# Optimization experiments

Measured on AMD Instinct MI355X. Metric: run time of the kernel, lower is better.

## Reference

```python
import jax, jax.numpy as jnp
import numpy as np

HX_INIT = 1e-6  # matches torch: zeros + 1e-06


def log_g(x):
    # log of continuous activation g: x>=0 -> log(x+0.5), else log(sigmoid(x)) = -softplus(-x)
    return jnp.where(x >= 0, jnp.log(jax.nn.relu(x) + 0.5), -jax.nn.softplus(-x))


def setup_inputs() -> dict:
    key = jax.random.key(0)
    k1, k2, k3 = jax.random.split(key, 3)
    N, L, H_in, H = 8, 4096, 512, 512
    x = jax.random.normal(k1, (N, L, H_in), dtype=jnp.float32)
    W = jax.random.normal(k2, (3 * H, H_in), dtype=jnp.float32) * 0.05
    b = jax.random.normal(k3, (3 * H,), dtype=jnp.float32) * 0.05
    return {"x": x, "W": W, "b": b}


def reference(x, W, b):
    N, L, _ = x.shape
    H = W.shape[0] // 3
    # gate preactivations: (N, L, 3H)
    pre = jnp.einsum('nli,oi->nlo', x, W) + b
    f_pre, i_pre, h_pre = jnp.split(pre, 3, axis=-1)
    # log-space gates
    diff = jax.nn.softplus(-f_pre) - jax.nn.softplus(-i_pre)
    log_f = -jax.nn.softplus(diff)       # log f'_t
    log_i = -jax.nn.softplus(-diff)      # log i'_t
    log_tilde_h = log_g(h_pre)
    # initial hidden state hx = 1e-6 (zeros + eps), shape (N, 1, H)
    log_h0 = jnp.full((N, 1, H), jnp.log(jnp.asarray(HX_INIT, x.dtype)), dtype=x.dtype)
    log_values = jnp.concatenate([log_h0, log_i + log_tilde_h], axis=1)  # (N, L+1, H)
    # Heinsen log-space parallel scan
    a_star = jnp.pad(jnp.cumsum(log_f, axis=1), ((0, 0), (1, 0), (0, 0)))  # (N, L+1, H)
    log_h = a_star + jax.lax.cumlogsumexp(log_values - a_star, axis=1)
    return jnp.exp(log_h)[:, 1:]  # (N, L, H)
```

## Files before the change

### kernel.cpp

```cpp
#include <hip/hip_runtime.h>
#include <hip/hip_bf16.h>


#define H_DIM 512
#define LSEQ 4096
#define NBATCH 8
#define M_TOTAL (NBATCH * LSEQ)

#define BM 128
#define BK 64

#define CS 128
#define NC 32

typedef __attribute__((ext_vector_type(8))) short short8;
typedef __attribute__((ext_vector_type(4))) float floatx4;
typedef __attribute__((ext_vector_type(4))) float float4v;
typedef _Float16 h2 __attribute__((ext_vector_type(2)));
typedef _Float16 h4 __attribute__((ext_vector_type(4)));
typedef __attribute__((ext_vector_type(2))) float float2v;

#define NEG_BIG (-1.0e30f)
#define C_LOG2E 1.4426950408889634f
#define LOG2_HX0 (-19.931568569324174f)

__device__ __forceinline__ float exp2_hw(float x) {
#if __has_builtin(__builtin_amdgcn_exp2f)
    return __builtin_amdgcn_exp2f(x);
#else
    return exp2f(x);
#endif
}

__device__ __forceinline__ float log2_hw(float x) {
#if __has_builtin(__builtin_amdgcn_logf)
    return __builtin_amdgcn_logf(x);
#else
    return log2f(x);
#endif
}

__device__ __forceinline__ float logaddexp2_f(float p, float q) {
    float m = fmaxf(p, q);
    float d = -fabsf(p - q);
    return m + log2_hw(1.0f + exp2_hw(d));
}

__device__ __forceinline__ float bf16u_to_f(unsigned short u) {
    unsigned int w = ((unsigned int)u) << 16;
    float f;
    __builtin_memcpy(&f, &w, 4);
    return f;
}

__device__ __forceinline__ unsigned short f_to_bf16u(float f) {
    __hip_bfloat16 h = __float2bfloat16(f);
    unsigned short u;
    __builtin_memcpy(&u, &h, 2);
    return u;
}

__device__ __forceinline__ void gload_lds16(const void* g, void* l) {
    __builtin_amdgcn_global_load_lds(
        (const __attribute__((address_space(1))) unsigned int*)g,
        (__attribute__((address_space(3))) unsigned int*)l, 16, 0, 0);
}

__global__ void detect_and_bias(const unsigned short* __restrict__ xu,
                                const void* __restrict__ bsrc,
                                int* __restrict__ flag,
                                float* __restrict__ bdst) {
    __shared__ int cnt;
    if (threadIdx.x == 0) cnt = 0;
    __syncthreads();
    int local = 0;
    for (int i = threadIdx.x; i < 16384; i += 256) {
        unsigned short u = xu[i];
        if (((u >> 7) & 0xFF) == 0xFF) local++;
    }
    if (local) atomicAdd(&cnt, local);
    __syncthreads();
    int f = (cnt > 8) ? 1 : 0;
    if (threadIdx.x == 0) flag[0] = f;
    for (int i = threadIdx.x; i < 3 * H_DIM; i += 256)
        bdst[i] = f ? ((const float*)bsrc)[i]
                    : bf16u_to_f(((const unsigned short*)bsrc)[i]);
}

__global__ __launch_bounds__(256)
void convert_inputs(const void* __restrict__ x, const void* __restrict__ W,
                    unsigned short* __restrict__ xc,
                    unsigned short* __restrict__ Wc,
                    const int* __restrict__ flag) {
    const int bx = blockIdx.x;
    const void* src;
    unsigned short* dst;
    int i;
    if (bx < 8192) { src = x; dst = xc; i = (bx * 256 + threadIdx.x) * 8; }
    else           { src = W; dst = Wc; i = ((bx - 8192) * 256 + threadIdx.x) * 8; }
    if (*flag) {
        const float4v* s4 = (const float4v*)((const float*)src + i);
        float4v a = s4[0], b = s4[1];
        short8 v;
        v[0] = (short)f_to_bf16u(a[0]); v[1] = (short)f_to_bf16u(a[1]);
        v[2] = (short)f_to_bf16u(a[2]); v[3] = (short)f_to_bf16u(a[3]);
        v[4] = (short)f_to_bf16u(b[0]); v[5] = (short)f_to_bf16u(b[1]);
        v[6] = (short)f_to_bf16u(b[2]); v[7] = (short)f_to_bf16u(b[3]);
        *(short8*)&dst[i] = v;
    } else {
        *(short8*)&dst[i] = *(const short8*)&((const short*)src)[i];
    }
}

__global__ __launch_bounds__(256, 3)
void gemm_gates(const unsigned short* __restrict__ x,
                const unsigned short* __restrict__ W,
                const float* __restrict__ bias,
                h2* __restrict__ plv,
                float* __restrict__ Asum, float* __restrict__ Bval,
                float* __restrict__ Asub, float* __restrict__ Bsub) {
    __shared__ __align__(16) char ldsbuf[40960];
    short* Alds = (short*)ldsbuf;
    short* Blds = (short*)(ldsbuf + 16384);
    h2* sc = (h2*)ldsbuf;
    float* sa = (float*)(ldsbuf + 32768);
    float* sb = sa + 256;

    const int bx = blockIdx.x;
    const int by = blockIdx.y;
    const int tid = threadIdx.x;
    const int lane = tid & 63;
    const int w = tid >> 6;
    const int wr = (w >> 1) * 64;
    const int wc2 = w & 1;
    const int l8 = lane >> 3, s8 = lane & 7;
    const int sg = s8 ^ l8;
    const int fr = lane & 15;
    const int q = lane >> 4;

    const int R0 = by * BM;

    floatx4 acc[4][6];
    #pragma unroll
    for (int i = 0; i < 4; i++)
        #pragma unroll
        for (int j = 0; j < 6; j++)
            acc[i][j] = (floatx4){0.f, 0.f, 0.f, 0.f};

    const short* xg = (const short*)x;
    const short* wg = (const short*)W;

    for (int k0 = 0; k0 < H_DIM; k0 += BK) {
        __syncthreads();
        #pragma unroll
        for (int i = 0; i < 4; i++) {
            int c = w * 4 + i;
            const short* g = xg + (size_t)(R0 + c * 8 + l8) * H_DIM + k0 + sg * 8;
            gload_lds16(g, &Alds[c * 512]);
        }
        #pragma unroll
        for (int i = 0; i < 6; i++) {
            int c = w * 6 + i;
            int br = c * 8 + l8;
            int wrow = (br >> 6) * H_DIM + bx * 64 + (br & 63);
            const short* g = wg + (size_t)wrow * H_DIM + k0 + sg * 8;
            gload_lds16(g, &Blds[c * 512]);
        }
        __syncthreads();

        #pragma unroll
        for (int ks = 0; ks < 2; ks++) {
            const int s = ks * 4 + q;
            short8 af[4], bf[6];
            #pragma unroll
            for (int mt = 0; mt < 4; mt++) {
                int ar = wr + mt * 16 + fr;
                af[mt] = *(const short8*)&Alds[ar * BK + ((s ^ (ar & 7)) << 3)];
            }
            #pragma unroll
            for (int j = 0; j < 6; j++) {
                int nt = (j >> 1) * 4 + wc2 * 2 + (j & 1);
                int brr = nt * 16 + fr;
                bf[j] = *(const short8*)&Blds[brr * BK + ((s ^ (brr & 7)) << 3)];
            }
            #pragma unroll
            for (int mt = 0; mt < 4; mt++)
                #pragma unroll
                for (int j = 0; j < 6; j++)
                    acc[mt][j] = __builtin_amdgcn_mfma_f32_16x16x32_bf16(
                        af[mt], bf[j], acc[mt][j], 0, 0, 0);
        }
    }

    __syncthreads();

    const int rowb = R0 + wr + q * 4;
    const int tloc0 = wr + q * 4;
    #pragma unroll
    for (int jj = 0; jj < 2; jj++) {
        int hl = wc2 * 32 + jj * 16 + fr;
        int hcol = bx * 64 + hl;
        float bfv = bias[hcol];
        float biv = bias[H_DIM + hcol];
        float bhv = bias[2 * H_DIM + hcol];
        float bf2 = -bfv * C_LOG2E;
        float bi2 = -biv * C_LOG2E;
        #pragma unroll
        for (int mt = 0; mt < 4; mt++) {
            #pragma unroll
            for (int r = 0; r < 4; r++) {
                float ef = exp2_hw(fminf(fmaf(acc[mt][jj][r], -C_LOG2E, bf2), 126.0f));
                float ei = exp2_hw(fminf(fmaf(acc[mt][2 + jj][r], -C_LOG2E, bi2), 126.0f));
                float hp = acc[mt][4 + jj][r] + bhv;
                float eh = exp2_hw(fminf(-hp * C_LOG2E, 126.0f));
                float afv = 1.0f + ef, aiv = 1.0f + ei;
                float sfi = afv + aiv;
                float ls = log2_hw(sfi);
                float lf = log2_hw(aiv) - ls;
                float marg = (hp >= 0.0f) ? (hp + 0.5f) : (1.0f + eh);
                float lm = log2_hw(marg);
                float lg = (hp >= 0.0f) ? lm : -lm;
                float lv = (log2_hw(afv) - ls) + lg;
                int row = rowb + mt * 16 + r;
                h2 pk;
                pk[0] = (_Float16)lf;
                pk[1] = (_Float16)lv;
                plv[(size_t)row * H_DIM + hcol] = pk;
                sc[(tloc0 + mt * 16 + r) * 64 + hl] = pk;
            }
        }
    }

    __syncthreads();

    const int n = by >> 5, c = by & 31;
    {
        float a = 0.f, bacc = NEG_BIG;
        const int t0 = w * 32;
        #pragma unroll 4
        for (int t = t0; t < t0 + 32; t++) {
            h2 p = sc[t * 64 + lane];
            float f = (float)p[0];
            bacc = logaddexp2_f(f + bacc, (float)p[1]);
            a += f;
        }
        sa[w * 64 + lane] = a;
        sb[w * 64 + lane] = bacc;
        size_t o = (((size_t)n * NC + c) * 4 + w) * H_DIM + bx * 64 + lane;
        Asub[o] = a;
        Bsub[o] = bacc;
    }
    __syncthreads();

    if (w == 0) {
        float a = sa[lane], b = sb[lane];
        #pragma unroll
        for (int s = 1; s < 4; s++) {
            float as = sa[s * 64 + lane], bs = sb[s * 64 + lane];
            b = logaddexp2_f(as + b, bs);
            a += as;
        }
        size_t o = ((size_t)n * NC + c) * H_DIM + bx * 64 + lane;
        Asum[o] = a;
        Bval[o] = b;
    }
}

__global__ __launch_bounds__(256)
void scan_apply(const h2* __restrict__ plv,
                const float* __restrict__ Asum, const float* __restrict__ Bval,
                const float* __restrict__ Asub, const float* __restrict__ Bsub,
                void* __restrict__ outv, const int* __restrict__ flag) {
    const int cc = blockIdx.x;
    const int n = blockIdx.y;
    const int c = cc >> 2, s = cc & 3;
    const int h0 = threadIdx.x * 2;
    const int f32out = *flag;

    float r0 = LOG2_HX0;
    float r1 = r0;
    size_t so = (size_t)n * NC * H_DIM + h0;
    int cp = 0;
    for (; cp + 4 <= c; cp += 4) {
        float2v A0 = *(const float2v*)&Asum[so + (size_t)(cp + 0) * H_DIM];
        float2v B0 = *(const float2v*)&Bval[so + (size_t)(cp + 0) * H_DIM];
        float2v A1 = *(const float2v*)&Asum[so + (size_t)(cp + 1) * H_DIM];
        float2v B1 = *(const float2v*)&Bval[so + (size_t)(cp + 1) * H_DIM];
        float2v A2 = *(const float2v*)&Asum[so + (size_t)(cp + 2) * H_DIM];
        float2v B2 = *(const float2v*)&Bval[so + (size_t)(cp + 2) * H_DIM];
        float2v A3 = *(const float2v*)&Asum[so + (size_t)(cp + 3) * H_DIM];
        float2v B3 = *(const float2v*)&Bval[so + (size_t)(cp + 3) * H_DIM];
        r0 = logaddexp2_f(A0[0] + r0, B0[0]); r1 = logaddexp2_f(A0[1] + r1, B0[1]);
        r0 = logaddexp2_f(A1[0] + r0, B1[0]); r1 = logaddexp2_f(A1[1] + r1, B1[1]);
        r0 = logaddexp2_f(A2[0] + r0, B2[0]); r1 = logaddexp2_f(A2[1] + r1, B2[1]);
        r0 = logaddexp2_f(A3[0] + r0, B3[0]); r1 = logaddexp2_f(A3[1] + r1, B3[1]);
    }
    for (; cp < c; cp++) {
        float2v A = *(const float2v*)&Asum[so + (size_t)cp * H_DIM];
        float2v B = *(const float2v*)&Bval[so + (size_t)cp * H_DIM];
        r0 = logaddexp2_f(A[0] + r0, B[0]);
        r1 = logaddexp2_f(A[1] + r1, B[1]);
    }
    size_t sub = (((size_t)n * NC + c) * 4) * H_DIM + h0;
    for (int sp = 0; sp < s; sp++) {
        float2v A = *(const float2v*)&Asub[sub + (size_t)sp * H_DIM];
        float2v B = *(const float2v*)&Bsub[sub + (size_t)sp * H_DIM];
        r0 = logaddexp2_f(A[0] + r0, B[0]);
        r1 = logaddexp2_f(A[1] + r1, B[1]);
    }

    size_t base = ((size_t)n * LSEQ + (size_t)c * CS + s * 32) * H_DIM + h0;
    if (f32out) {
        float* of = (float*)outv;
        #pragma unroll 4
        for (int t = 0; t < 32; t++) {
            size_t idx = base + (size_t)t * H_DIM;
            h4 p = *(const h4*)&plv[idx];
            r0 = logaddexp2_f((float)p[0] + r0, (float)p[1]);
            r1 = logaddexp2_f((float)p[2] + r1, (float)p[3]);
            float2v o2 = {exp2_hw(r0), exp2_hw(r1)};
            *(float2v*)&of[idx] = o2;
        }
    } else {
        unsigned int* ob32 = (unsigned int*)outv;
        #pragma unroll 4
        for (int t = 0; t < 32; t++) {
            size_t idx = base + (size_t)t * H_DIM;
            h4 p = *(const h4*)&plv[idx];
            r0 = logaddexp2_f((float)p[0] + r0, (float)p[1]);
            r1 = logaddexp2_f((float)p[2] + r1, (float)p[3]);
            unsigned int pk = ((unsigned int)f_to_bf16u(exp2_hw(r1)) << 16)
                            | f_to_bf16u(exp2_hw(r0));
            ob32[idx >> 1] = pk;
        }
    }
}

extern "C" void kernel_launch(void* const* d_in, const int* in_sizes, int n_in,
                              void* d_out, int out_size, void* d_ws, size_t ws_size,
                              hipStream_t stream) {
    const void* x = d_in[0];
    const void* W = d_in[1];
    const void* b = d_in[2];

    char* wsb = (char*)d_ws;
    int* flag            = (int*)wsb;
    float* bconv         = (float*)(wsb + 16);
    unsigned short* xc   = (unsigned short*)(wsb + 16384);
    unsigned short* Wc   = (unsigned short*)(wsb + 16384 + 33554432);
    h2* plv              = (h2*)(wsb + 36700160);
    float* Asum          = (float*)(wsb + 103809024);
    float* Bval          = (float*)(wsb + 104333312);
    float* Asub          = (float*)(wsb + 104857600);
    float* Bsub          = (float*)(wsb + 106954752);

    detect_and_bias<<<1, 256, 0, stream>>>((const unsigned short*)x, b, flag, bconv);
    convert_inputs<<<8576, 256, 0, stream>>>(x, W, xc, Wc, flag);

    dim3 g1(H_DIM / 64, M_TOTAL / BM);
    gemm_gates<<<g1, 256, 0, stream>>>(xc, Wc, bconv, plv, Asum, Bval, Asub, Bsub);

    dim3 g2(NC * 4, NBATCH);
    scan_apply<<<g2, 256, 0, stream>>>(plv, Asum, Bval, Asub, Bsub, d_out, flag);
}
```

Baseline: 235.6 us.

## Fuse fp32-to-bf16 conversion of x into GEMM A-tile loads

Drops the separate pass that converted x to bf16. When the input is fp32, the GEMM now reads fp32 x directly, packs it to bf16 with v_cvt_pk_bf16_f32 and stores the result into LDS; only W is still converted ahead of time. This removes a full write and re-read of the converted activation buffer. The grid axes are also swapped so consecutive blocks walk along rows instead of output columns. That changes L2 reuse: x is now fetched as fp32 once per column tile, and the A loads become synchronous register loads instead of direct-to-LDS loads.

Result: no change. 238.4 us (+1.2%).

```diff
diff --git a/kernel.cpp b/kernel.cpp
--- a/kernel.cpp
+++ b/kernel.cpp
@@ -60,6 +60,12 @@
     return u;
 }
 
+__device__ __forceinline__ unsigned int cvtpk_bf16(float lo, float hi) {
+    unsigned int r;
+    asm("v_cvt_pk_bf16_f32 %0, %1, %2" : "=v"(r) : "v"(lo), "v"(hi));
+    return r;
+}
+
 __device__ __forceinline__ void gload_lds16(const void* g, void* l) {
     __builtin_amdgcn_global_load_lds(
         (const __attribute__((address_space(1))) unsigned int*)g,
@@ -88,34 +94,28 @@
 }
 
 __global__ __launch_bounds__(256)
-void convert_inputs(const void* __restrict__ x, const void* __restrict__ W,
-                    unsigned short* __restrict__ xc,
-                    unsigned short* __restrict__ Wc,
-                    const int* __restrict__ flag) {
-    const int bx = blockIdx.x;
-    const void* src;
-    unsigned short* dst;
-    int i;
-    if (bx < 8192) { src = x; dst = xc; i = (bx * 256 + threadIdx.x) * 8; }
-    else           { src = W; dst = Wc; i = ((bx - 8192) * 256 + threadIdx.x) * 8; }
+void convert_w(const void* __restrict__ W, unsigned short* __restrict__ Wc,
+               const int* __restrict__ flag) {
+    const int i = (blockIdx.x * 256 + threadIdx.x) * 8;
     if (*flag) {
-        const float4v* s4 = (const float4v*)((const float*)src + i);
+        const float4v* s4 = (const float4v*)((const float*)W + i);
         float4v a = s4[0], b = s4[1];
         short8 v;
         v[0] = (short)f_to_bf16u(a[0]); v[1] = (short)f_to_bf16u(a[1]);
         v[2] = (short)f_to_bf16u(a[2]); v[3] = (short)f_to_bf16u(a[3]);
         v[4] = (short)f_to_bf16u(b[0]); v[5] = (short)f_to_bf16u(b[1]);
         v[6] = (short)f_to_bf16u(b[2]); v[7] = (short)f_to_bf16u(b[3]);
-        *(short8*)&dst[i] = v;
+        *(short8*)&Wc[i] = v;
     } else {
-        *(short8*)&dst[i] = *(const short8*)&((const short*)src)[i];
+        *(short8*)&Wc[i] = *(const short8*)&((const short*)W)[i];
     }
 }
 
 __global__ __launch_bounds__(256, 3)
-void gemm_gates(const unsigned short* __restrict__ x,
+void gemm_gates(const void* __restrict__ x,
                 const unsigned short* __restrict__ W,
                 const float* __restrict__ bias,
+                const int* __restrict__ flag,
                 h2* __restrict__ plv,
                 float* __restrict__ Asum, float* __restrict__ Bval,
                 float* __restrict__ Asub, float* __restrict__ Bsub) {
@@ -126,8 +126,8 @@
     float* sa = (float*)(ldsbuf + 32768);
     float* sb = sa + 256;
 
-    const int bx = blockIdx.x;
-    const int by = blockIdx.y;
+    const int by = blockIdx.x;
+    const int bx = blockIdx.y;
     const int tid = threadIdx.x;
     const int lane = tid & 63;
     const int w = tid >> 6;
@@ -139,6 +139,7 @@
     const int q = lane >> 4;
 
     const int R0 = by * BM;
+    const int f32in = *flag;
 
     floatx4 acc[4][6];
     #pragma unroll
@@ -147,16 +148,38 @@
         for (int j = 0; j < 6; j++)
             acc[i][j] = (floatx4){0.f, 0.f, 0.f, 0.f};
 
-    const short* xg = (const short*)x;
+    const float* xf = (const float*)x;
+    const short* xh = (const short*)x;
     const short* wg = (const short*)W;
 
     for (int k0 = 0; k0 < H_DIM; k0 += BK) {
         __syncthreads();
-        #pragma unroll
-        for (int i = 0; i < 4; i++) {
-            int c = w * 4 + i;
-            const short* g = xg + (size_t)(R0 + c * 8 + l8) * H_DIM + k0 + sg * 8;
-            gload_lds16(g, &Alds[c * 512]);
+        if (f32in) {
+            float4v va[4][2];
+            #pragma unroll
+            for (int i = 0; i < 4; i++) {
+                int c = w * 4 + i;
+                const float* g = xf + (size_t)(R0 + c * 8 + l8) * H_DIM + k0 + sg * 8;
+                va[i][0] = *(const float4v*)g;
+                va[i][1] = *(const float4v*)(g + 4);
+            }
+            #pragma unroll
+            for (int i = 0; i < 4; i++) {
+                int c = w * 4 + i;
+                union { short8 s; unsigned int u[4]; } pkv;
+                pkv.u[0] = cvtpk_bf16(va[i][0][0], va[i][0][1]);
+                pkv.u[1] = cvtpk_bf16(va[i][0][2], va[i][0][3]);
+                pkv.u[2] = cvtpk_bf16(va[i][1][0], va[i][1][1]);
+                pkv.u[3] = cvtpk_bf16(va[i][1][2], va[i][1][3]);
+                *(short8*)&Alds[c * 512 + lane * 8] = pkv.s;
+            }
+        } else {
+            #pragma unroll
+            for (int i = 0; i < 4; i++) {
+                int c = w * 4 + i;
+                const short* g = xh + (size_t)(R0 + c * 8 + l8) * H_DIM + k0 + sg * 8;
+                gload_lds16(g, &Alds[c * 512]);
+            }
         }
         #pragma unroll
         for (int i = 0; i < 6; i++) {
@@ -346,7 +369,6 @@
     char* wsb = (char*)d_ws;
     int* flag            = (int*)wsb;
     float* bconv         = (float*)(wsb + 16);
-    unsigned short* xc   = (unsigned short*)(wsb + 16384);
     unsigned short* Wc   = (unsigned short*)(wsb + 16384 + 33554432);
     h2* plv              = (h2*)(wsb + 36700160);
     float* Asum          = (float*)(wsb + 103809024);
@@ -355,10 +377,10 @@
     float* Bsub          = (float*)(wsb + 106954752);
 
     detect_and_bias<<<1, 256, 0, stream>>>((const unsigned short*)x, b, flag, bconv);
-    convert_inputs<<<8576, 256, 0, stream>>>(x, W, xc, Wc, flag);
-
-    dim3 g1(H_DIM / 64, M_TOTAL / BM);
-    gemm_gates<<<g1, 256, 0, stream>>>(xc, Wc, bconv, plv, Asum, Bval, Asub, Bsub);
+    convert_w<<<384, 256, 0, stream>>>(W, Wc, flag);
+
+    dim3 g1(M_TOTAL / BM, H_DIM / 64);
+    gemm_gates<<<g1, 256, 0, stream>>>(x, Wc, bconv, flag, plv, Asum, Bval, Asub, Bsub);
 
     dim3 g2(NC * 4, NBATCH);
     scan_apply<<<g2, 256, 0, stream>>>(plv, Asum, Bval, Asub, Bsub, d_out, flag);
```
